# Kernel tuning notes

Measured on AMD Instinct MI355X. Metric: run time of the kernel, lower is better.

The kernel has to match this reference:

```python
import jax, jax.numpy as jnp
import numpy as np

BATCH = 4096
IN_SIZES = [1024, 1024, 1024, 1024]
EMB = 2048  # embracement_size


def setup_inputs() -> dict:
    key = jax.random.key(0)
    keys = jax.random.split(key, 3 * len(IN_SIZES))
    inp = {}
    for i, d in enumerate(IN_SIZES):
        inp[f"x{i}"] = jax.random.normal(keys[3 * i], (BATCH, d), dtype=jnp.float32)
        # Linear params (Kaiming-ish scale)
        inp[f"W{i}"] = jax.random.normal(keys[3 * i + 1], (d, EMB), dtype=jnp.float32) / np.sqrt(d)
        inp[f"b{i}"] = jax.random.normal(keys[3 * i + 2], (EMB,), dtype=jnp.float32) * 0.01
    return inp


def _sample_indices(batch, num_feats, emb):
    # availabilities=None, selection_probabilities=None -> uniform p over modalities
    # multinomial(p, num_samples=emb, replacement=True) == categorical over log p
    logits = jnp.zeros((batch, num_feats), dtype=jnp.float32)  # uniform
    k = jax.random.key(42)
    # shape (emb, batch) broadcasts against logits batch shape (batch,)
    idx = jax.random.categorical(k, logits, axis=-1, shape=(emb, batch))
    return idx.T  # [batch, emb]


def reference(x0, W0, b0, x1, W1, b1, x2, W2, b2, x3, W3, b3):
    xs = [x0, x1, x2, x3]
    Ws = [W0, W1, W2, W3]
    bs = [b0, b1, b2, b3]
    # docking: Linear + ReLU per modality -> [batch, EMB, num_feats]
    dock = jnp.stack([jax.nn.relu(x @ W + b) for x, W, b in zip(xs, Ws, bs)], axis=-1)
    B, E, F = dock.shape
    idx = _sample_indices(B, F, E)  # [B, E] int32
    # gather along modality axis (replaces one-hot multiply-sum)
    out = jnp.take_along_axis(dock, idx[:, :, None], axis=-1)[..., 0]
    return out  # [batch, EMB]
```

## Files before the change

kernel.cpp:

```cpp
#include <hip/hip_runtime.h>
#include <stdint.h>


typedef short short8 __attribute__((ext_vector_type(8)));
typedef float floatx4 __attribute__((ext_vector_type(4)));

#define B_DIM 4096
#define K_DIM 1024
#define E_DIM 2048

__device__ __forceinline__ uint16_t f2bf(float x) {
  uint32_t u = __float_as_uint(x);
  u += 0x7FFFu + ((u >> 16) & 1u);
  return (uint16_t)(u >> 16);
}

__device__ __forceinline__ void threefry(uint32_t x0, uint32_t x1,
                                         uint32_t& o0, uint32_t& o1) {
  const uint32_t ks0 = 0u;
  const uint32_t ks1 = 42u;
  const uint32_t ks2 = 0x1BD11BDAu ^ 42u;
  x0 += ks0; x1 += ks1;
#define TF_R(r) { x0 += x1; x1 = (x1 << r) | (x1 >> (32 - r)); x1 ^= x0; }
  TF_R(13) TF_R(15) TF_R(26) TF_R(6)
  x0 += ks1; x1 += ks2 + 1u;
  TF_R(17) TF_R(29) TF_R(16) TF_R(24)
  x0 += ks2; x1 += ks0 + 2u;
  TF_R(13) TF_R(15) TF_R(26) TF_R(6)
  x0 += ks0; x1 += ks1 + 3u;
  TF_R(17) TF_R(29) TF_R(16) TF_R(24)
  x0 += ks1; x1 += ks2 + 4u;
  TF_R(13) TF_R(15) TF_R(26) TF_R(6)
  x0 += ks2; x1 += ks0 + 5u;
#undef TF_R
  o0 = x0; o1 = x1;
}

__device__ __forceinline__ uint32_t pick_modality(uint32_t e, uint32_t b) {
  uint32_t base = ((e << 12) + b) << 2;
  uint32_t best = 0, bi = 0;
#pragma unroll
  for (uint32_t f = 0; f < 4; ++f) {
    uint32_t y0, y1;
    threefry(0u, base + f, y0, y1);
    uint32_t m = (y0 ^ y1) >> 9;
    if (f == 0) best = m;
    else if (m > best) { best = m; bi = f; }
  }
  return bi;
}

__global__ __launch_bounds__(256) void convert_x(
    const float* __restrict__ x0, const float* __restrict__ x1,
    const float* __restrict__ x2, const float* __restrict__ x3,
    uint16_t* __restrict__ xb) {
  int f = blockIdx.z;
  const float* x = (f == 0) ? x0 : (f == 1) ? x1 : (f == 2) ? x2 : x3;
  size_t i = ((size_t)blockIdx.x * 256 + threadIdx.x) * 4;
  float4 v = *(const float4*)(x + i);
  union { uint16_t h[4]; uint64_t q; } p;
  p.h[0] = f2bf(v.x); p.h[1] = f2bf(v.y);
  p.h[2] = f2bf(v.z); p.h[3] = f2bf(v.w);
  *(uint64_t*)(xb + (size_t)f * B_DIM * K_DIM + i) = p.q;
}

__global__ __launch_bounds__(256) void convert_w(
    const float* __restrict__ W0, const float* __restrict__ W1,
    const float* __restrict__ W2, const float* __restrict__ W3,
    uint16_t* __restrict__ Wt) {
  __shared__ float tile[32][33];
  int f = blockIdx.z;
  const float* W = (f == 0) ? W0 : (f == 1) ? W1 : (f == 2) ? W2 : W3;
  int e0 = blockIdx.x * 32, k0 = blockIdx.y * 32;
  int tx = threadIdx.x, ty = threadIdx.y;
#pragma unroll
  for (int i = 0; i < 4; ++i)
    tile[ty + i * 8][tx] = W[(size_t)(k0 + ty + i * 8) * E_DIM + e0 + tx];
  __syncthreads();
  uint16_t* dst = Wt + (size_t)f * E_DIM * K_DIM;
#pragma unroll
  for (int i = 0; i < 4; ++i)
    dst[(size_t)(e0 + ty + i * 8) * K_DIM + k0 + tx] = f2bf(tile[tx][ty + i * 8]);
}

__device__ __forceinline__ void async16(const uint16_t* g, uint16_t* lds) {
  __builtin_amdgcn_global_load_lds(
      (const __attribute__((address_space(1))) void*)g,
      (__attribute__((address_space(3))) void*)lds, 16, 0, 0);
}

__global__ __launch_bounds__(256, 2) void gemm_fused(
    const uint16_t* __restrict__ Ab, const uint16_t* __restrict__ Bbt,
    const float* __restrict__ bias0, const float* __restrict__ bias1,
    const float* __restrict__ bias2, const float* __restrict__ bias3,
    float* __restrict__ out) {
  __shared__ uint16_t As[128 * 32];
  __shared__ uint16_t Bs[128 * 32];

  const int tid = threadIdx.x;
  const int w = tid >> 6;
  const int l = tid & 63;
  const int mBase = blockIdx.y * 128;
  const int nBase = blockIdx.x * 128;

  const int wm = (w >> 1) * 64, wn = (w & 1) * 64;
  const int ar = l >> 2, ac8 = l & 3;
  const int fr = l & 15, fq = l >> 4;

  float bv[4][4];
#pragma unroll
  for (int ni = 0; ni < 4; ++ni) {
    int col = nBase + wn + ni * 16 + fr;
    bv[0][ni] = bias0[col]; bv[1][ni] = bias1[col];
    bv[2][ni] = bias2[col]; bv[3][ni] = bias3[col];
  }

  uint32_t idxbits[4];
#pragma unroll
  for (int ni = 0; ni < 4; ++ni) {
    uint32_t e = nBase + wn + ni * 16 + fr;
    uint32_t word = 0;
#pragma unroll 1
    for (int mi = 0; mi < 4; ++mi) {
      uint32_t b0 = mBase + wm + mi * 16 + fq * 4;
#pragma unroll 1
      for (int r = 0; r < 4; ++r) {
        uint32_t bi = pick_modality(e, b0 + r);
        word |= bi << (2 * (mi * 4 + r));
      }
    }
    idxbits[ni] = word;
  }

  floatx4 res[4][4] = {};

#pragma unroll 1
  for (int f = 0; f < 4; ++f) {
    const uint16_t* A = Ab  + (size_t)f * B_DIM * K_DIM + (size_t)mBase * K_DIM;
    const uint16_t* B = Bbt + (size_t)f * E_DIM * K_DIM + (size_t)nBase * K_DIM;

    floatx4 acc[4][4] = {};
    for (int k0 = 0; k0 < K_DIM; k0 += 32) {
      #pragma unroll
      for (int t = 0; t < 2; ++t) {
        int c = w * 2 + t;
        async16(A + (size_t)(c * 16 + ar) * K_DIM + k0 + ac8 * 8, &As[c * 512]);
        async16(B + (size_t)(c * 16 + ar) * K_DIM + k0 + ac8 * 8, &Bs[c * 512]);
      }
      __syncthreads();

      short8 a[4], b[4];
      #pragma unroll
      for (int mi = 0; mi < 4; ++mi)
        a[mi] = *(const short8*)&As[(wm + mi * 16 + fr) * 32 + fq * 8];
      #pragma unroll
      for (int ni = 0; ni < 4; ++ni)
        b[ni] = *(const short8*)&Bs[(wn + ni * 16 + fr) * 32 + fq * 8];
      #pragma unroll
      for (int mi = 0; mi < 4; ++mi)
        #pragma unroll
        for (int ni = 0; ni < 4; ++ni)
          acc[mi][ni] = __builtin_amdgcn_mfma_f32_16x16x32_bf16(
              a[mi], b[ni], acc[mi][ni], 0, 0, 0);
      __syncthreads();
    }

    #pragma unroll
    for (int ni = 0; ni < 4; ++ni) {
      float bvf = bv[f][ni];
      uint32_t word = idxbits[ni];
      #pragma unroll
      for (int mi = 0; mi < 4; ++mi)
        #pragma unroll
        for (int r = 0; r < 4; ++r) {
          uint32_t sel = (word >> (2 * (mi * 4 + r))) & 3u;
          if (sel == (uint32_t)f) res[mi][ni][r] = acc[mi][ni][r] + bvf;
        }
    }
  }

#pragma unroll
  for (int ni = 0; ni < 4; ++ni) {
    int col = nBase + wn + ni * 16 + fr;
#pragma unroll
    for (int mi = 0; mi < 4; ++mi) {
      int row0 = mBase + wm + mi * 16 + fq * 4;
#pragma unroll
      for (int r = 0; r < 4; ++r) {
        float o = res[mi][ni][r];
        out[(size_t)(row0 + r) * E_DIM + col] = o > 0.f ? o : 0.f;
      }
    }
  }
}

extern "C" void kernel_launch(void* const* d_in, const int* in_sizes, int n_in,
                              void* d_out, int out_size, void* d_ws, size_t ws_size,
                              hipStream_t stream) {
  const float* x[4]; const float* W[4]; const float* bs[4];
  for (int f = 0; f < 4; ++f) {
    x[f]  = (const float*)d_in[3 * f + 0];
    W[f]  = (const float*)d_in[3 * f + 1];
    bs[f] = (const float*)d_in[3 * f + 2];
  }
  char* ws = (char*)d_ws;
  uint16_t* xb = (uint16_t*)ws;
  uint16_t* Wt = (uint16_t*)(ws + (size_t)32 * 1024 * 1024);
  float* out = (float*)d_out;

  convert_x<<<dim3(4096, 1, 4), dim3(256), 0, stream>>>(x[0], x[1], x[2], x[3], xb);
  convert_w<<<dim3(64, 32, 4), dim3(32, 8), 0, stream>>>(W[0], W[1], W[2], W[3], Wt);
  gemm_fused<<<dim3(E_DIM / 128, B_DIM / 128), dim3(256), 0, stream>>>(
      xb, Wt, bs[0], bs[1], bs[2], bs[3], out);
}
```

Measured before the change: 312.8 us.

## Precompute modality indices in a separate kernel and load packed bits in GEMM

```diff
diff --git a/kernel.cpp b/kernel.cpp
--- a/kernel.cpp
+++ b/kernel.cpp
@@ -36,18 +36,25 @@
   o0 = x0; o1 = x1;
 }
 
-__device__ __forceinline__ uint32_t pick_modality(uint32_t e, uint32_t b) {
-  uint32_t base = ((e << 12) + b) << 2;
-  uint32_t best = 0, bi = 0;
-#pragma unroll
-  for (uint32_t f = 0; f < 4; ++f) {
-    uint32_t y0, y1;
-    threefry(0u, base + f, y0, y1);
-    uint32_t m = (y0 ^ y1) >> 9;
-    if (f == 0) best = m;
-    else if (m > best) { best = m; bi = f; }
-  }
-  return bi;
+__global__ __launch_bounds__(256) void idx_kernel(uint32_t* __restrict__ idx2) {
+  uint32_t tid = blockIdx.x * 256u + threadIdx.x;
+  uint32_t base = tid << 6;
+  uint32_t word = 0;
+#pragma unroll 2
+  for (int j = 0; j < 16; ++j) {
+    uint32_t c = base + 4u * j;
+    uint32_t best = 0, bi = 0;
+#pragma unroll
+    for (uint32_t f = 0; f < 4; ++f) {
+      uint32_t y0, y1;
+      threefry(0u, c + f, y0, y1);
+      uint32_t m = (y0 ^ y1) >> 9;
+      if (f == 0) best = m;
+      else if (m > best) { best = m; bi = f; }
+    }
+    word |= bi << (2 * j);
+  }
+  idx2[tid] = word;
 }
 
 __global__ __launch_bounds__(256) void convert_x(
@@ -91,6 +98,7 @@
 
 __global__ __launch_bounds__(256, 2) void gemm_fused(
     const uint16_t* __restrict__ Ab, const uint16_t* __restrict__ Bbt,
+    const uint32_t* __restrict__ idx2,
     const float* __restrict__ bias0, const float* __restrict__ bias1,
     const float* __restrict__ bias2, const float* __restrict__ bias3,
     float* __restrict__ out) {
@@ -107,29 +115,14 @@
   const int ar = l >> 2, ac8 = l & 3;
   const int fr = l & 15, fq = l >> 4;
 
-  float bv[4][4];
+  const int b_hi0 = (mBase + wm) >> 4;
+  uint32_t iw[4][4];
 #pragma unroll
   for (int ni = 0; ni < 4; ++ni) {
     int col = nBase + wn + ni * 16 + fr;
-    bv[0][ni] = bias0[col]; bv[1][ni] = bias1[col];
-    bv[2][ni] = bias2[col]; bv[3][ni] = bias3[col];
-  }
-
-  uint32_t idxbits[4];
-#pragma unroll
-  for (int ni = 0; ni < 4; ++ni) {
-    uint32_t e = nBase + wn + ni * 16 + fr;
-    uint32_t word = 0;
-#pragma unroll 1
-    for (int mi = 0; mi < 4; ++mi) {
-      uint32_t b0 = mBase + wm + mi * 16 + fq * 4;
-#pragma unroll 1
-      for (int r = 0; r < 4; ++r) {
-        uint32_t bi = pick_modality(e, b0 + r);
-        word |= bi << (2 * (mi * 4 + r));
-      }
-    }
-    idxbits[ni] = word;
+#pragma unroll
+    for (int mi = 0; mi < 4; ++mi)
+      iw[ni][mi] = idx2[(size_t)col * (B_DIM / 16) + b_hi0 + mi];
   }
 
   floatx4 res[4][4] = {};
@@ -165,17 +158,20 @@
       __syncthreads();
     }
 
+    const float* bias = (f == 0) ? bias0 : (f == 1) ? bias1
+                      : (f == 2) ? bias2 : bias3;
     #pragma unroll
     for (int ni = 0; ni < 4; ++ni) {
-      float bvf = bv[f][ni];
-      uint32_t word = idxbits[ni];
-      #pragma unroll
-      for (int mi = 0; mi < 4; ++mi)
+      float bvf = bias[nBase + wn + ni * 16 + fr];
+      #pragma unroll
+      for (int mi = 0; mi < 4; ++mi) {
+        uint32_t wd = iw[ni][mi];
         #pragma unroll
         for (int r = 0; r < 4; ++r) {
-          uint32_t sel = (word >> (2 * (mi * 4 + r))) & 3u;
+          uint32_t sel = (wd >> (2 * (fq * 4 + r))) & 3u;
           if (sel == (uint32_t)f) res[mi][ni][r] = acc[mi][ni][r] + bvf;
         }
+      }
     }
   }
 
@@ -188,7 +184,8 @@
 #pragma unroll
       for (int r = 0; r < 4; ++r) {
         float o = res[mi][ni][r];
-        out[(size_t)(row0 + r) * E_DIM + col] = o > 0.f ? o : 0.f;
+        __builtin_nontemporal_store(o > 0.f ? o : 0.f,
+                                    &out[(size_t)(row0 + r) * E_DIM + col]);
       }
     }
   }
@@ -204,12 +201,14 @@
     bs[f] = (const float*)d_in[3 * f + 2];
   }
   char* ws = (char*)d_ws;
-  uint16_t* xb = (uint16_t*)ws;
-  uint16_t* Wt = (uint16_t*)(ws + (size_t)32 * 1024 * 1024);
+  uint16_t* xb  = (uint16_t*)ws;
+  uint16_t* Wt  = (uint16_t*)(ws + (size_t)32 * 1024 * 1024);
+  uint32_t* idx2 = (uint32_t*)(ws + (size_t)48 * 1024 * 1024);
   float* out = (float*)d_out;
 
+  idx_kernel<<<dim3(2048), dim3(256), 0, stream>>>(idx2);
   convert_x<<<dim3(4096, 1, 4), dim3(256), 0, stream>>>(x[0], x[1], x[2], x[3], xb);
   convert_w<<<dim3(64, 32, 4), dim3(32, 8), 0, stream>>>(W[0], W[1], W[2], W[3], Wt);
   gemm_fused<<<dim3(E_DIM / 128, B_DIM / 128), dim3(256), 0, stream>>>(
-      xb, Wt, bs[0], bs[1], bs[2], bs[3], out);
-}
+      xb, Wt, idx2, bs[0], bs[1], bs[2], bs[3], out);
+}
```

New measurement: 309.2 us. Within noise of the previous version (-1.1%).
